# Performance work log

Hardware: AMD Instinct MI355X
Metric: run time of the kernel (lower is better)

## Reference

```python
import jax, jax.numpy as jnp
import numpy as np

B, N, HID, H, FFN, E = 1, 50000, 96, 8, 384, 800000
D = HID // H
SCALE = float(np.sqrt(D))


def _layernorm(x, g, b, eps=1e-5):
    mu = jnp.mean(x, axis=-1, keepdims=True)
    var = jnp.var(x, axis=-1, keepdims=True)
    return (x - mu) * jax.lax.rsqrt(var + eps) * g + b


def setup_inputs() -> dict:
    key = jax.random.key(0)
    ks = jax.random.split(key, 20)
    std = 0.02
    inp = {
        "x": jax.random.normal(ks[0], (B, N, HID), dtype=jnp.float32),
        "edge_index": jax.random.randint(ks[1], (2, E), 0, B * N, dtype=jnp.int32),
        "ln1_g": jnp.ones((HID,), jnp.float32),
        "ln1_b": jnp.zeros((HID,), jnp.float32),
        "Wq": jax.random.normal(ks[2], (HID, HID), jnp.float32) * std,
        "bq": jnp.zeros((HID,), jnp.float32),
        "Wk": jax.random.normal(ks[3], (HID, HID), jnp.float32) * std,
        "bk": jnp.zeros((HID,), jnp.float32),
        "Wv": jax.random.normal(ks[4], (HID, HID), jnp.float32) * std,
        "bv": jnp.zeros((HID,), jnp.float32),
        "Wo": jax.random.normal(ks[5], (HID, HID), jnp.float32) * std,
        "bo": jnp.zeros((HID,), jnp.float32),
        "ln2_g": jnp.ones((HID,), jnp.float32),
        "ln2_b": jnp.zeros((HID,), jnp.float32),
        "W1": jax.random.normal(ks[6], (HID, FFN), jnp.float32) * std,
        "b1": jnp.zeros((FFN,), jnp.float32),
        "W2": jax.random.normal(ks[7], (FFN, HID), jnp.float32) * std,
        "b2": jnp.zeros((HID,), jnp.float32),
    }
    return inp


def _sparse_attn(q, k, v, edge_index):
    # q,k,v: [B*N, H, D]; edge_index: [2, E]
    src_idx = edge_index[0].astype(jnp.int32)
    dst_idx = edge_index[1].astype(jnp.int32)
    src = k[src_idx]                                # [E, H, D]
    dest = q[dst_idx]                               # [E, H, D]
    score = jnp.sum(src * dest, axis=-1, keepdims=True) / SCALE  # [E, H, 1]
    score = jnp.exp(jnp.clip(score, -5.0, 5.0))
    msg = v[src_idx] * score                        # [E, H, D]
    wV = jax.ops.segment_sum(msg, dst_idx, num_segments=B * N)   # [B*N, H, D]
    Z = jax.ops.segment_sum(score, dst_idx, num_segments=B * N)  # [B*N, H, 1]
    return wV / (Z + 1e-6)


def reference(x, edge_index, ln1_g, ln1_b, Wq, bq, Wk, bk, Wv, bv, Wo, bo,
              ln2_g, ln2_b, W1, b1, W2, b2):
    # --- self-attention block ---
    y = _layernorm(x, ln1_g, ln1_b)                 # [B, N, HID]
    q = (y @ Wq + bq).reshape(B * N, H, D)
    k = (y @ Wk + bk).reshape(B * N, H, D)
    v = (y @ Wv + bv).reshape(B * N, H, D)
    a = _sparse_attn(q, k, v, edge_index)           # [B*N, H, D]
    a = a.reshape(B, N, HID)
    y = a @ Wo + bo
    x = x + y
    # --- FFN block ---
    y = _layernorm(x, ln2_g, ln2_b)
    y = jax.nn.gelu(y @ W1 + b1, approximate=False)
    y = y @ W2 + b2
    return x + y
```

## Files before the change

### kernel.cpp

```cpp
#include <hip/hip_runtime.h>
#include <hip/hip_bf16.h>
#include <math.h>

#define NN 50000
#define HIDD 96
#define NH 8
#define HD 12
#define FFND 384
#define NE 800000
#define NB 98
#define BSTRIDE 12288

#define INV_SCALE 0.28867513459481287f
#define LOG2E 1.4426950408889634f

typedef short short8 __attribute__((ext_vector_type(8)));
typedef float f32x4 __attribute__((ext_vector_type(4)));
typedef float f32x2 __attribute__((ext_vector_type(2)));

__device__ __forceinline__ float bf2f(unsigned short u) {
    union { unsigned int i; float f; } c;
    c.i = ((unsigned int)u) << 16;
    return c.f;
}

__global__ __launch_bounds__(256) void prep(
    int* __restrict__ gcursor,
    const float* __restrict__ Wq, const float* __restrict__ Wk,
    const float* __restrict__ Wv, const float* __restrict__ Wo,
    const float* __restrict__ W1, const float* __restrict__ W2,
    __hip_bfloat16* __restrict__ wbuf,
    const float* __restrict__ x, const float* __restrict__ g1,
    const float* __restrict__ b1, __hip_bfloat16* __restrict__ ybf) {
    int b = blockIdx.x;
    int t = threadIdx.x;
    if (b == 0) {
        if (t < 128) gcursor[t] = t * BSTRIDE;
        return;
    }
    if (b < 433) {
        int idx = b - 1;
        const float* W; __hip_bfloat16* D; int K, N; int i;
        if (idx < 144)      { W = W1; D = wbuf + 36864; K = 96;  N = 384; i = idx * 256 + t; }
        else if (idx < 288) { W = W2; D = wbuf + 73728; K = 384; N = 96;  i = (idx - 144) * 256 + t; }
        else {
            int slab = (idx - 288) / 36;
            W = (slab == 0) ? Wq : (slab == 1) ? Wk : (slab == 2) ? Wv : Wo;
            D = wbuf + slab * 9216; K = 96; N = 96;
            i = ((idx - 288) % 36) * 256 + t;
        }
        if (i < K * N) {
            int n = i / K, k = i % K;
            D[i] = __float2bfloat16(W[k * N + n]);
        }
    } else {
        int row = (b - 433) * 4 + (t >> 6);
        int lane = t & 63;
        if (row >= NN) return;
        const float* xr = x + (size_t)row * HIDD;
        float v0 = xr[lane];
        float v1 = (lane < 32) ? xr[64 + lane] : 0.0f;
        float s = v0 + v1, q = v0 * v0 + v1 * v1;
#pragma unroll
        for (int o = 32; o > 0; o >>= 1) {
            s += __shfl_xor(s, o);
            q += __shfl_xor(q, o);
        }
        float mean = s * (1.0f / 96.0f);
        float var = q * (1.0f / 96.0f) - mean * mean;
        float rs = rsqrtf(var + 1e-5f);
        __hip_bfloat16* yr = ybf + (size_t)row * HIDD;
        yr[lane] = __float2bfloat16((v0 - mean) * rs * g1[lane] + b1[lane]);
        if (lane < 32)
            yr[64 + lane] = __float2bfloat16((v1 - mean) * rs * g1[64 + lane] + b1[64 + lane]);
    }
}

__global__ __launch_bounds__(256) void scatter_qkv(
    const int* __restrict__ ei, int* __restrict__ gcursor,
    unsigned int* __restrict__ ebuf,
    const __hip_bfloat16* __restrict__ A, const __hip_bfloat16* __restrict__ wbuf,
    const float* __restrict__ bq, const float* __restrict__ bk,
    const float* __restrict__ bv,
    __hip_bfloat16* __restrict__ qbf, unsigned char* __restrict__ kv) {
    int b = blockIdx.x;
    int t = threadIdx.x;
    if (b < 391) {
        __shared__ int lcount[128];
        __shared__ int lbase[128];
        int e0 = b * 2048;
        if (t < 128) lcount[t] = 0;
        __syncthreads();
        int rank[8], dsts[8], srcv[8];
#pragma unroll
        for (int i = 0; i < 8; i++) {
            int e = e0 + t + i * 256;
            if (e < NE) {
                srcv[i] = ei[e];
                int d = ei[NE + e];
                dsts[i] = d;
                rank[i] = atomicAdd(&lcount[d >> 9], 1);
            } else dsts[i] = -1;
        }
        __syncthreads();
        if (t < 128) lbase[t] = lcount[t] ? atomicAdd(&gcursor[t], lcount[t]) : 0;
        __syncthreads();
#pragma unroll
        for (int i = 0; i < 8; i++) {
            if (dsts[i] >= 0) {
                int bk_ = dsts[i] >> 9;
                ebuf[lbase[bk_] + rank[i]] =
                    ((unsigned int)dsts[i] << 16) | (unsigned int)srcv[i];
            }
        }
    } else {
        __shared__ __hip_bfloat16 Bs[96][104];
        int xb = b - 391;
        int lane = t & 63, wave = t >> 6;
        int row0 = xb * 128 + wave * 32;
        int lr = lane & 15, kg = lane >> 4;
        bool val0 = (row0 + 16 <= NN);
        bool val1 = (row0 + 32 <= NN);
        int ra0 = val0 ? row0 : 0;
        int ra1 = val1 ? (row0 + 16) : 0;
        short8 a0[3], a1[3];
#pragma unroll
        for (int kc = 0; kc < 3; kc++) {
            a0[kc] = *(const short8*)&A[(size_t)(ra0 + lr) * 96 + kc * 32 + kg * 8];
            a1[kc] = *(const short8*)&A[(size_t)(ra1 + lr) * 96 + kc * 32 + kg * 8];
        }
        for (int y = 0; y < 3; y++) {
            const __hip_bfloat16* slab = wbuf + y * 9216;
            for (int i = t * 8; i < 96 * 96; i += 256 * 8) {
                int r = i / 96, c = i % 96;
                *(short8*)&Bs[r][c] = *(const short8*)&slab[r * 96 + c];
            }
            __syncthreads();
            f32x4 acc[2][6];
#pragma unroll
            for (int f = 0; f < 2; f++)
#pragma unroll
                for (int ct = 0; ct < 6; ct++) acc[f][ct] = (f32x4){0.f, 0.f, 0.f, 0.f};
#pragma unroll
            for (int kc = 0; kc < 3; kc++) {
#pragma unroll
                for (int ct = 0; ct < 6; ct++) {
                    short8 bf_ = *(const short8*)&Bs[ct * 16 + lr][kc * 32 + kg * 8];
                    acc[0][ct] = __builtin_amdgcn_mfma_f32_16x16x32_bf16(a0[kc], bf_, acc[0][ct], 0, 0, 0);
                    acc[1][ct] = __builtin_amdgcn_mfma_f32_16x16x32_bf16(a1[kc], bf_, acc[1][ct], 0, 0, 0);
                }
            }
            const float* bias = (y == 0) ? bq : (y == 1) ? bk : bv;
            int koff = (y == 2) ? 12 : 0;
#pragma unroll
            for (int f = 0; f < 2; f++) {
                if (f == 0 ? !val0 : !val1) continue;
                int crow = row0 + f * 16 + kg * 4;
#pragma unroll
                for (int ct = 0; ct < 6; ct++) {
                    int col = ct * 16 + lr;
                    float bb = bias[col];
#pragma unroll
                    for (int r = 0; r < 4; r++) {
                        float o = acc[f][ct][r] + bb;
                        if (y == 0) {
                            qbf[(size_t)(crow + r) * HIDD + col] = __float2bfloat16(o);
                        } else {
                            unsigned int enc =
                                (unsigned int)__builtin_amdgcn_cvt_pk_fp8_f32(o, o, 0, false);
                            kv[(size_t)(crow + r) * 192 + (col / 12) * 24 + koff + (col % 12)]
                                = (unsigned char)(enc & 0xffu);
                        }
                    }
                }
            }
            __syncthreads();
        }
    }
}

__global__ __launch_bounds__(1024) void bucket_build(
    const unsigned int* __restrict__ ebuf, const int* __restrict__ gcursor,
    uint2* __restrict__ rowrange, unsigned short* __restrict__ srcs) {
    __shared__ int cnt[512];
    int b = blockIdx.x;
    int t = threadIdx.x;
    int n0 = b * 512;
    int beg = b * BSTRIDE;
    int end = gcursor[b];
    if (t < 512) cnt[t] = 0;
    __syncthreads();
    for (int e = beg + t; e < end; e += 1024)
        atomicAdd(&cnt[(ebuf[e] >> 16) - n0], 1);
    __syncthreads();
    int my = (t < 512) ? cnt[t] : 0;
    for (int off = 1; off < 512; off <<= 1) {
        int v = (t >= off && t < 512) ? cnt[t - off] : 0;
        __syncthreads();
        if (t < 512) cnt[t] += v;
        __syncthreads();
    }
    int excl = (t > 0 && t < 512) ? cnt[t - 1] : 0;
    int base = beg + excl;
    if (t < 512 && n0 + t < NN)
        rowrange[n0 + t] = make_uint2((unsigned)base, (unsigned)(base + my));
    __syncthreads();
    if (t < 512) cnt[t] = base;
    __syncthreads();
    for (int e = beg + t; e < end; e += 1024) {
        unsigned int u = ebuf[e];
        int pos = atomicAdd(&cnt[(u >> 16) - n0], 1);
        srcs[pos] = (unsigned short)(u & 0xffffu);
    }
}

__global__ __launch_bounds__(256) void proj_ln(
    const __hip_bfloat16* __restrict__ A, const __hip_bfloat16* __restrict__ BT,
    const float* __restrict__ bias, const float* __restrict__ R,
    const float* __restrict__ g2, const float* __restrict__ b2v,
    __hip_bfloat16* __restrict__ x2, __hip_bfloat16* __restrict__ ybf) {
    constexpr int K = 96;
    __shared__ __hip_bfloat16 Bs[96][K + 8];
    int t = threadIdx.x;
    int lane = t & 63, wave = t >> 6;
    int row0 = blockIdx.x * 128 + wave * 32;
    int lr = lane & 15, kg = lane >> 4;
    bool val0 = (row0 + 16 <= NN);
    bool val1 = (row0 + 32 <= NN);
    int ra0 = val0 ? row0 : 0;
    int ra1 = val1 ? (row0 + 16) : 0;
    const __hip_bfloat16* A0 = A + (size_t)(ra0 + lr) * K + kg * 8;
    const __hip_bfloat16* A1 = A + (size_t)(ra1 + lr) * K + kg * 8;
    f32x4 acc[2][6];
#pragma unroll
    for (int f = 0; f < 2; f++)
#pragma unroll
        for (int ct = 0; ct < 6; ct++) acc[f][ct] = (f32x4){0.f, 0.f, 0.f, 0.f};

    for (int i = t * 8; i < 96 * K; i += 256 * 8) {
        int r = i / K, c = i % K;
        *(short8*)&Bs[r][c] = *(const short8*)&BT[(size_t)r * K + c];
    }
    __syncthreads();
#pragma unroll
    for (int kc = 0; kc < K; kc += 32) {
        short8 a0 = *(const short8*)(A0 + kc);
        short8 a1 = *(const short8*)(A1 + kc);
#pragma unroll
        for (int ct = 0; ct < 6; ct++) {
            short8 bf_ = *(const short8*)&Bs[ct * 16 + lr][kc + kg * 8];
            acc[0][ct] = __builtin_amdgcn_mfma_f32_16x16x32_bf16(a0, bf_, acc[0][ct], 0, 0, 0);
            acc[1][ct] = __builtin_amdgcn_mfma_f32_16x16x32_bf16(a1, bf_, acc[1][ct], 0, 0, 0);
        }
    }

    float bo_[6], gv[6], bv_[6];
#pragma unroll
    for (int ct = 0; ct < 6; ct++) {
        int col = ct * 16 + lr;
        bo_[ct] = bias[col];
        gv[ct]  = g2[col];
        bv_[ct] = b2v[col];
    }
#pragma unroll
    for (int f = 0; f < 2; f++) {
        if (f == 0 ? !val0 : !val1) continue;
        int crow = row0 + f * 16 + kg * 4;
#pragma unroll
        for (int r = 0; r < 4; r++) {
            int row = crow + r;
            float o[6], s1 = 0.f, s2 = 0.f;
#pragma unroll
            for (int ct = 0; ct < 6; ct++) {
                int col = ct * 16 + lr;
                float val = acc[f][ct][r] + bo_[ct] + R[(size_t)row * 96 + col];
                o[ct] = val; s1 += val; s2 += val * val;
            }
#pragma unroll
            for (int m = 1; m < 16; m <<= 1) {
                s1 += __shfl_xor(s1, m);
                s2 += __shfl_xor(s2, m);
            }
            float mu = s1 * (1.0f / 96.0f);
            float var = s2 * (1.0f / 96.0f) - mu * mu;
            float rs = rsqrtf(var + 1e-5f);
#pragma unroll
            for (int ct = 0; ct < 6; ct++) {
                int col = ct * 16 + lr;
                x2[(size_t)row * 96 + col] = __float2bfloat16(o[ct]);
                ybf[(size_t)row * 96 + col] =
                    __float2bfloat16((o[ct] - mu) * rs * gv[ct] + bv_[ct]);
            }
        }
    }
}

__global__ __launch_bounds__(256) void ffn1_p(
    const __hip_bfloat16* __restrict__ ybf, const __hip_bfloat16* __restrict__ W1T,
    const float* __restrict__ b1, __hip_bfloat16* __restrict__ hbf) {
    __shared__ __hip_bfloat16 Bs[96][104];
    int t = threadIdx.x, lane = t & 63, wave = t >> 6;
    int lr = lane & 15, kg = lane >> 4;
    int row0 = blockIdx.x * 64 + wave * 16;
    bool valid = (row0 + 16 <= NN);
    int ra = valid ? row0 : 0;
    short8 af[3];
#pragma unroll
    for (int kc = 0; kc < 3; kc++)
        af[kc] = *(const short8*)&ybf[(size_t)(ra + lr) * 96 + kc * 32 + kg * 8];

    for (int s = 0; s < 4; s++) {
        const __hip_bfloat16* slab = W1T + (size_t)s * 96 * 96;
        for (int i = t * 8; i < 96 * 96; i += 256 * 8) {
            int r = i / 96, c = i % 96;
            *(short8*)&Bs[r][c] = *(const short8*)&slab[r * 96 + c];
        }
        __syncthreads();
        f32x4 acc[6];
#pragma unroll
        for (int ct = 0; ct < 6; ct++) acc[ct] = (f32x4){0.f, 0.f, 0.f, 0.f};
#pragma unroll
        for (int kc = 0; kc < 3; kc++) {
#pragma unroll
            for (int ct = 0; ct < 6; ct++) {
                short8 bf_ = *(const short8*)&Bs[ct * 16 + lr][kc * 32 + kg * 8];
                acc[ct] = __builtin_amdgcn_mfma_f32_16x16x32_bf16(af[kc], bf_, acc[ct], 0, 0, 0);
            }
        }
        if (valid) {
            int crow = row0 + kg * 4;
#pragma unroll
            for (int ct = 0; ct < 6; ct++) {
                int col = s * 96 + ct * 16 + lr;
                float bb = b1[col];
#pragma unroll
                for (int r = 0; r < 4; r++) {
                    float o = acc[ct][r] + bb;
                    o = 0.5f * o * (1.0f + erff(o * 0.70710678118654752f));
                    hbf[(size_t)(crow + r) * FFND + col] = __float2bfloat16(o);
                }
            }
        }
        __syncthreads();
    }
}

__global__ __launch_bounds__(256) void ffn2_p(
    const __hip_bfloat16* __restrict__ hbf, const __hip_bfloat16* __restrict__ W2T,
    const float* __restrict__ b2v, const __hip_bfloat16* __restrict__ x2,
    float* __restrict__ out) {
    __shared__ __hip_bfloat16 Bs[4][48][104];
    int t = threadIdx.x, lane = t & 63, wave = t >> 6;
    int lr = lane & 15, kg = lane >> 4;
    int row0 = blockIdx.x * 64 + wave * 16;
    bool valid = (row0 + 16 <= NN);
    int ra = valid ? row0 : 0;
    short8 hf[12];
#pragma unroll
    for (int kc = 0; kc < 12; kc++)
        hf[kc] = *(const short8*)&hbf[(size_t)(ra + lr) * FFND + kc * 32 + kg * 8];

    for (int ch = 0; ch < 2; ch++) {
        const __hip_bfloat16* wslab = W2T + (size_t)ch * 48 * 384;
        for (int i = t * 8; i < 48 * 384; i += 256 * 8) {
            int r = i / 384, c = i % 384;
            *(short8*)&Bs[c / 96][r][c % 96] = *(const short8*)&wslab[(size_t)r * 384 + c];
        }
        __syncthreads();
        f32x4 acc[3];
#pragma unroll
        for (int ct = 0; ct < 3; ct++) acc[ct] = (f32x4){0.f, 0.f, 0.f, 0.f};
#pragma unroll
        for (int kc = 0; kc < 12; kc++) {
#pragma unroll
            for (int ct = 0; ct < 3; ct++) {
                short8 bf_ = *(const short8*)&Bs[kc / 3][ct * 16 + lr][(kc % 3) * 32 + kg * 8];
                acc[ct] = __builtin_amdgcn_mfma_f32_16x16x32_bf16(hf[kc], bf_, acc[ct], 0, 0, 0);
            }
        }
        if (valid) {
            int crow = row0 + kg * 4;
#pragma unroll
            for (int ct = 0; ct < 3; ct++) {
                int col = ch * 48 + ct * 16 + lr;
                float bb = b2v[col];
#pragma unroll
                for (int r = 0; r < 4; r++) {
                    float o = acc[ct][r] + bb
                            + __bfloat162float(x2[(size_t)(crow + r) * 96 + col]);
                    out[(size_t)(crow + r) * 96 + col] = o;
                }
            }
        }
        __syncthreads();
    }
}

__global__ __launch_bounds__(256) void attn_gather(
    const __hip_bfloat16* __restrict__ qbf, const unsigned char* __restrict__ kv,
    const uint2* __restrict__ rowrange, const unsigned short* __restrict__ srcs,
    __hip_bfloat16* __restrict__ abf) {
    int wave = (blockIdx.x * blockDim.x + threadIdx.x) >> 6;
    int lane = threadIdx.x & 63;
    if (wave >= NN) return;
    int dst = wave;
    int h = lane & 7;
    int eslot = lane >> 3;
    float qf[12];
    {
        const uint2* qp = (const uint2*)(qbf + (size_t)dst * HIDD + h * HD);
        uint2 u0 = qp[0], u1 = qp[1], u2 = qp[2];
        unsigned int w[6] = {u0.x, u0.y, u1.x, u1.y, u2.x, u2.y};
#pragma unroll
        for (int i = 0; i < 6; i++) {
            qf[2 * i]     = bf2f((unsigned short)(w[i] & 0xffffu));
            qf[2 * i + 1] = bf2f((unsigned short)(w[i] >> 16));
        }
    }
    uint2 rr = rowrange[dst];
    int beg = (int)rr.x, end = (int)rr.y;
    float acc[12];
#pragma unroll
    for (int i = 0; i < 12; i++) acc[i] = 0.0f;
    float zz = 0.0f;

    int e = beg + eslot;
    bool has = e < end;
    uint2 cA, cB, cC;
    if (has) {
        int src = (int)srcs[e];
        const uint2* kp = (const uint2*)(kv + (size_t)src * 192 + h * 24);
        cA = kp[0]; cB = kp[1]; cC = kp[2];
    }
    while (has) {
        int en = e + 8;
        bool hasn = en < end;
        uint2 nA, nB, nC;
        if (hasn) {
            int srcn = (int)srcs[en];
            const uint2* kp = (const uint2*)(kv + (size_t)srcn * 192 + h * 24);
            nA = kp[0]; nB = kp[1]; nC = kp[2];
        }
        f32x2 p;
        float dot = 0.0f;
        p = __builtin_amdgcn_cvt_pk_f32_fp8(cA.x, false); dot += p[0] * qf[0]  + p[1] * qf[1];
        p = __builtin_amdgcn_cvt_pk_f32_fp8(cA.x, true);  dot += p[0] * qf[2]  + p[1] * qf[3];
        p = __builtin_amdgcn_cvt_pk_f32_fp8(cA.y, false); dot += p[0] * qf[4]  + p[1] * qf[5];
        p = __builtin_amdgcn_cvt_pk_f32_fp8(cA.y, true);  dot += p[0] * qf[6]  + p[1] * qf[7];
        p = __builtin_amdgcn_cvt_pk_f32_fp8(cB.x, false); dot += p[0] * qf[8]  + p[1] * qf[9];
        p = __builtin_amdgcn_cvt_pk_f32_fp8(cB.x, true);  dot += p[0] * qf[10] + p[1] * qf[11];
        float s = fminf(fmaxf(dot * INV_SCALE, -5.0f), 5.0f);
        float sc = exp2f(s * LOG2E);
        p = __builtin_amdgcn_cvt_pk_f32_fp8(cB.y, false); acc[0]  += p[0] * sc; acc[1]  += p[1] * sc;
        p = __builtin_amdgcn_cvt_pk_f32_fp8(cB.y, true);  acc[2]  += p[0] * sc; acc[3]  += p[1] * sc;
        p = __builtin_amdgcn_cvt_pk_f32_fp8(cC.x, false); acc[4]  += p[0] * sc; acc[5]  += p[1] * sc;
        p = __builtin_amdgcn_cvt_pk_f32_fp8(cC.x, true);  acc[6]  += p[0] * sc; acc[7]  += p[1] * sc;
        p = __builtin_amdgcn_cvt_pk_f32_fp8(cC.y, false); acc[8]  += p[0] * sc; acc[9]  += p[1] * sc;
        p = __builtin_amdgcn_cvt_pk_f32_fp8(cC.y, true);  acc[10] += p[0] * sc; acc[11] += p[1] * sc;
        zz += sc;
        cA = nA; cB = nB; cC = nC;
        e = en; has = hasn;
    }
#pragma unroll
    for (int m = 8; m < 64; m <<= 1) {
#pragma unroll
        for (int i = 0; i < 12; i++) acc[i] += __shfl_xor(acc[i], m);
        zz += __shfl_xor(zz, m);
    }
    if (eslot == 0) {
        float inv = 1.0f / (zz + 1e-6f);
        __hip_bfloat16* ar = abf + (size_t)dst * HIDD + h * HD;
#pragma unroll
        for (int i = 0; i < 12; i++) ar[i] = __float2bfloat16(acc[i] * inv);
    }
}

extern "C" void kernel_launch(void* const* d_in, const int* in_sizes, int n_in,
                              void* d_out, int out_size, void* d_ws, size_t ws_size,
                              hipStream_t stream) {
    const float* x     = (const float*)d_in[0];
    const int*   ei    = (const int*)d_in[1];
    const float* ln1_g = (const float*)d_in[2];
    const float* ln1_b = (const float*)d_in[3];
    const float* Wq    = (const float*)d_in[4];
    const float* bq    = (const float*)d_in[5];
    const float* Wk    = (const float*)d_in[6];
    const float* bk    = (const float*)d_in[7];
    const float* Wv    = (const float*)d_in[8];
    const float* bv    = (const float*)d_in[9];
    const float* Wo    = (const float*)d_in[10];
    const float* bo    = (const float*)d_in[11];
    const float* ln2_g = (const float*)d_in[12];
    const float* ln2_b = (const float*)d_in[13];
    const float* W1    = (const float*)d_in[14];
    const float* b1    = (const float*)d_in[15];
    const float* W2    = (const float*)d_in[16];
    const float* b2    = (const float*)d_in[17];
    float* out = (float*)d_out;

    float* ws = (float*)d_ws;
    const size_t NF = (size_t)NN * HIDD;
    __hip_bfloat16* qbf = (__hip_bfloat16*)ws;
    unsigned char*  kv  = (unsigned char*)(ws + NF / 2);
    __hip_bfloat16* abf = (__hip_bfloat16*)(ws + NF / 2 + NF);
    __hip_bfloat16* hbf = (__hip_bfloat16*)ws;
    __hip_bfloat16* x2  = (__hip_bfloat16*)(ws + 2 * NF);
    __hip_bfloat16* ybf = (__hip_bfloat16*)(ws + 2 * NF + NF / 2);
    int* ibase = (int*)(ws + 3 * NF);
    uint2* rowrange = (uint2*)ibase;
    unsigned short* srcs = (unsigned short*)(ibase + 2 * NN);
    int* gcursor = ibase + 2 * NN + (NB * BSTRIDE + 1) / 2;
    unsigned int* ebuf = (unsigned int*)(gcursor + 128);
    __hip_bfloat16* wbuf = (__hip_bfloat16*)(ws + 3 * NF + NF / 2);
    __hip_bfloat16* WoT = wbuf + 27648;
    __hip_bfloat16* W1T = wbuf + 36864;
    __hip_bfloat16* W2T = wbuf + 73728;

    const int MT = (NN + 127) / 128;
    const int FT = (NN + 63) / 64;

    prep<<<433 + 12500, 256, 0, stream>>>(gcursor, Wq, Wk, Wv, Wo, W1, W2, wbuf,
                                          x, ln1_g, ln1_b, ybf);
    scatter_qkv<<<391 + MT, 256, 0, stream>>>(ei, gcursor, ebuf,
                                              ybf, wbuf, bq, bk, bv, qbf, kv);
    bucket_build<<<NB, 1024, 0, stream>>>(ebuf, gcursor, rowrange, srcs);
    attn_gather<<<(NN + 3) / 4, 256, 0, stream>>>(qbf, kv, rowrange, srcs, abf);
    proj_ln<<<MT, 256, 0, stream>>>(abf, WoT, bo, x, ln2_g, ln2_b, x2, ybf);
    ffn1_p<<<FT, 256, 0, stream>>>(ybf, W1T, b1, hbf);
    ffn2_p<<<FT, 256, 0, stream>>>(hbf, W2T, b2, x2, out);
}
```

Measured before the change: 134.1 us.

## Regroup pipeline stages and store FFN hidden activations as fp8

The edge scatter moves into the prep kernel, and the bucket build is merged with the QKV projection into one 512-thread kernel. This drops a launch, and the QKV GEMM can overlap with the bucket build. The gcursor init becomes a memset with relative offsets. The FFN hidden activations are now written as fp8 and expanded to bf16 in ffn2, which halves that intermediate traffic at the cost of lower precision.

```diff
diff --git a/kernel.cpp b/kernel.cpp
--- a/kernel.cpp
+++ b/kernel.cpp
@@ -24,8 +24,26 @@
     return c.f;
 }
 
-__global__ __launch_bounds__(256) void prep(
-    int* __restrict__ gcursor,
+__device__ __forceinline__ short f2bf_exact(float f) {
+    return (short)(__float_as_uint(f) >> 16);
+}
+
+__device__ __forceinline__ short8 fp8x8_to_bf16x8(uint2 u) {
+    f32x2 p0 = __builtin_amdgcn_cvt_pk_f32_fp8(u.x, false);
+    f32x2 p1 = __builtin_amdgcn_cvt_pk_f32_fp8(u.x, true);
+    f32x2 p2 = __builtin_amdgcn_cvt_pk_f32_fp8(u.y, false);
+    f32x2 p3 = __builtin_amdgcn_cvt_pk_f32_fp8(u.y, true);
+    short8 r;
+    r[0] = f2bf_exact(p0[0]); r[1] = f2bf_exact(p0[1]);
+    r[2] = f2bf_exact(p1[0]); r[3] = f2bf_exact(p1[1]);
+    r[4] = f2bf_exact(p2[0]); r[5] = f2bf_exact(p2[1]);
+    r[6] = f2bf_exact(p3[0]); r[7] = f2bf_exact(p3[1]);
+    return r;
+}
+
+__global__ __launch_bounds__(256) void prep2(
+    const int* __restrict__ ei, int* __restrict__ gcursor,
+    unsigned int* __restrict__ ebuf,
     const float* __restrict__ Wq, const float* __restrict__ Wk,
     const float* __restrict__ Wv, const float* __restrict__ Wo,
     const float* __restrict__ W1, const float* __restrict__ W2,
@@ -34,12 +52,36 @@
     const float* __restrict__ b1, __hip_bfloat16* __restrict__ ybf) {
     int b = blockIdx.x;
     int t = threadIdx.x;
-    if (b == 0) {
-        if (t < 128) gcursor[t] = t * BSTRIDE;
-        return;
-    }
-    if (b < 433) {
-        int idx = b - 1;
+    if (b < 391) {
+        __shared__ int lcount[128];
+        __shared__ int lbase[128];
+        int e0 = b * 2048;
+        if (t < 128) lcount[t] = 0;
+        __syncthreads();
+        int rank[8], dsts[8], srcv[8];
+#pragma unroll
+        for (int i = 0; i < 8; i++) {
+            int e = e0 + t + i * 256;
+            if (e < NE) {
+                srcv[i] = ei[e];
+                int d = ei[NE + e];
+                dsts[i] = d;
+                rank[i] = atomicAdd(&lcount[d >> 9], 1);
+            } else dsts[i] = -1;
+        }
+        __syncthreads();
+        if (t < 128) lbase[t] = lcount[t] ? atomicAdd(&gcursor[t], lcount[t]) : 0;
+        __syncthreads();
+#pragma unroll
+        for (int i = 0; i < 8; i++) {
+            if (dsts[i] >= 0) {
+                int bk_ = dsts[i] >> 9;
+                ebuf[bk_ * BSTRIDE + lbase[bk_] + rank[i]] =
+                    ((unsigned int)dsts[i] << 16) | (unsigned int)srcv[i];
+            }
+        }
+    } else if (b < 823) {
+        int idx = b - 391;
         const float* W; __hip_bfloat16* D; int K, N; int i;
         if (idx < 144)      { W = W1; D = wbuf + 36864; K = 96;  N = 384; i = idx * 256 + t; }
         else if (idx < 288) { W = W2; D = wbuf + 73728; K = 384; N = 96;  i = (idx - 144) * 256 + t; }
@@ -54,7 +96,7 @@
             D[i] = __float2bfloat16(W[k * N + n]);
         }
     } else {
-        int row = (b - 433) * 4 + (t >> 6);
+        int row = (b - 823) * 4 + (t >> 6);
         int lane = t & 63;
         if (row >= NN) return;
         const float* xr = x + (size_t)row * HIDD;
@@ -76,93 +118,85 @@
     }
 }
 
-__global__ __launch_bounds__(256) void scatter_qkv(
-    const int* __restrict__ ei, int* __restrict__ gcursor,
-    unsigned int* __restrict__ ebuf,
+__global__ __launch_bounds__(512) void build_qkv(
+    const unsigned int* __restrict__ ebuf, const int* __restrict__ gcursor,
+    uint2* __restrict__ rowrange, unsigned short* __restrict__ srcs,
     const __hip_bfloat16* __restrict__ A, const __hip_bfloat16* __restrict__ wbuf,
     const float* __restrict__ bq, const float* __restrict__ bk,
     const float* __restrict__ bv,
     __hip_bfloat16* __restrict__ qbf, unsigned char* __restrict__ kv) {
+    __shared__ int cnt[512];
+    __shared__ __hip_bfloat16 Bs[96][104];
     int b = blockIdx.x;
     int t = threadIdx.x;
-    if (b < 391) {
-        __shared__ int lcount[128];
-        __shared__ int lbase[128];
-        int e0 = b * 2048;
-        if (t < 128) lcount[t] = 0;
-        __syncthreads();
-        int rank[8], dsts[8], srcv[8];
-#pragma unroll
-        for (int i = 0; i < 8; i++) {
-            int e = e0 + t + i * 256;
-            if (e < NE) {
-                srcv[i] = ei[e];
-                int d = ei[NE + e];
-                dsts[i] = d;
-                rank[i] = atomicAdd(&lcount[d >> 9], 1);
-            } else dsts[i] = -1;
-        }
-        __syncthreads();
-        if (t < 128) lbase[t] = lcount[t] ? atomicAdd(&gcursor[t], lcount[t]) : 0;
-        __syncthreads();
-#pragma unroll
-        for (int i = 0; i < 8; i++) {
-            if (dsts[i] >= 0) {
-                int bk_ = dsts[i] >> 9;
-                ebuf[lbase[bk_] + rank[i]] =
-                    ((unsigned int)dsts[i] << 16) | (unsigned int)srcv[i];
-            }
+    if (b < NB) {
+        int n0 = b * 512;
+        int beg = b * BSTRIDE;
+        int end = beg + gcursor[b];
+        cnt[t] = 0;
+        __syncthreads();
+        for (int e = beg + t; e < end; e += 512)
+            atomicAdd(&cnt[(ebuf[e] >> 16) - n0], 1);
+        __syncthreads();
+        int my = cnt[t];
+        for (int off = 1; off < 512; off <<= 1) {
+            int v = (t >= off) ? cnt[t - off] : 0;
+            __syncthreads();
+            cnt[t] += v;
+            __syncthreads();
+        }
+        int excl = (t > 0) ? cnt[t - 1] : 0;
+        int base = beg + excl;
+        if (n0 + t < NN)
+            rowrange[n0 + t] = make_uint2((unsigned)base, (unsigned)(base + my));
+        __syncthreads();
+        cnt[t] = base;
+        __syncthreads();
+        for (int e = beg + t; e < end; e += 512) {
+            unsigned int u = ebuf[e];
+            int pos = atomicAdd(&cnt[(u >> 16) - n0], 1);
+            srcs[pos] = (unsigned short)(u & 0xffffu);
         }
     } else {
-        __shared__ __hip_bfloat16 Bs[96][104];
-        int xb = b - 391;
+        int xb = b - NB;
         int lane = t & 63, wave = t >> 6;
-        int row0 = xb * 128 + wave * 32;
+        int row0 = xb * 128 + wave * 16;
         int lr = lane & 15, kg = lane >> 4;
-        bool val0 = (row0 + 16 <= NN);
-        bool val1 = (row0 + 32 <= NN);
-        int ra0 = val0 ? row0 : 0;
-        int ra1 = val1 ? (row0 + 16) : 0;
-        short8 a0[3], a1[3];
-#pragma unroll
-        for (int kc = 0; kc < 3; kc++) {
-            a0[kc] = *(const short8*)&A[(size_t)(ra0 + lr) * 96 + kc * 32 + kg * 8];
-            a1[kc] = *(const short8*)&A[(size_t)(ra1 + lr) * 96 + kc * 32 + kg * 8];
-        }
+        bool valid = (row0 + 16 <= NN);
+        int ra = valid ? row0 : 0;
+        short8 af[3];
+#pragma unroll
+        for (int kc = 0; kc < 3; kc++)
+            af[kc] = *(const short8*)&A[(size_t)(ra + lr) * 96 + kc * 32 + kg * 8];
         for (int y = 0; y < 3; y++) {
             const __hip_bfloat16* slab = wbuf + y * 9216;
-            for (int i = t * 8; i < 96 * 96; i += 256 * 8) {
+            for (int i = t * 8; i < 96 * 96; i += 512 * 8) {
                 int r = i / 96, c = i % 96;
                 *(short8*)&Bs[r][c] = *(const short8*)&slab[r * 96 + c];
             }
             __syncthreads();
-            f32x4 acc[2][6];
-#pragma unroll
-            for (int f = 0; f < 2; f++)
-#pragma unroll
-                for (int ct = 0; ct < 6; ct++) acc[f][ct] = (f32x4){0.f, 0.f, 0.f, 0.f};
+            f32x4 acc[6];
+#pragma unroll
+            for (int ct = 0; ct < 6; ct++) acc[ct] = (f32x4){0.f, 0.f, 0.f, 0.f};
 #pragma unroll
             for (int kc = 0; kc < 3; kc++) {
 #pragma unroll
                 for (int ct = 0; ct < 6; ct++) {
                     short8 bf_ = *(const short8*)&Bs[ct * 16 + lr][kc * 32 + kg * 8];
-                    acc[0][ct] = __builtin_amdgcn_mfma_f32_16x16x32_bf16(a0[kc], bf_, acc[0][ct], 0, 0, 0);
-                    acc[1][ct] = __builtin_amdgcn_mfma_f32_16x16x32_bf16(a1[kc], bf_, acc[1][ct], 0, 0, 0);
+                    acc[ct] = __builtin_amdgcn_mfma_f32_16x16x32_bf16(af[kc], bf_, acc[ct], 0, 0, 0);
                 }
             }
-            const float* bias = (y == 0) ? bq : (y == 1) ? bk : bv;
-            int koff = (y == 2) ? 12 : 0;
-#pragma unroll
-            for (int f = 0; f < 2; f++) {
-                if (f == 0 ? !val0 : !val1) continue;
-                int crow = row0 + f * 16 + kg * 4;
+            if (valid) {
+                const float* bias = (y == 0) ? bq : (y == 1) ? bk : bv;
+                int koff = (y == 2) ? 12 : 0;
+                int crow = row0 + kg * 4;
 #pragma unroll
                 for (int ct = 0; ct < 6; ct++) {
                     int col = ct * 16 + lr;
                     float bb = bias[col];
 #pragma unroll
                     for (int r = 0; r < 4; r++) {
-                        float o = acc[f][ct][r] + bb;
+                        float o = acc[ct][r] + bb;
                         if (y == 0) {
                             qbf[(size_t)(crow + r) * HIDD + col] = __float2bfloat16(o);
                         } else {
@@ -176,41 +210,6 @@
             }
             __syncthreads();
         }
-    }
-}
-
-__global__ __launch_bounds__(1024) void bucket_build(
-    const unsigned int* __restrict__ ebuf, const int* __restrict__ gcursor,
-    uint2* __restrict__ rowrange, unsigned short* __restrict__ srcs) {
-    __shared__ int cnt[512];
-    int b = blockIdx.x;
-    int t = threadIdx.x;
-    int n0 = b * 512;
-    int beg = b * BSTRIDE;
-    int end = gcursor[b];
-    if (t < 512) cnt[t] = 0;
-    __syncthreads();
-    for (int e = beg + t; e < end; e += 1024)
-        atomicAdd(&cnt[(ebuf[e] >> 16) - n0], 1);
-    __syncthreads();
-    int my = (t < 512) ? cnt[t] : 0;
-    for (int off = 1; off < 512; off <<= 1) {
-        int v = (t >= off && t < 512) ? cnt[t - off] : 0;
-        __syncthreads();
-        if (t < 512) cnt[t] += v;
-        __syncthreads();
-    }
-    int excl = (t > 0 && t < 512) ? cnt[t - 1] : 0;
-    int base = beg + excl;
-    if (t < 512 && n0 + t < NN)
-        rowrange[n0 + t] = make_uint2((unsigned)base, (unsigned)(base + my));
-    __syncthreads();
-    if (t < 512) cnt[t] = base;
-    __syncthreads();
-    for (int e = beg + t; e < end; e += 1024) {
-        unsigned int u = ebuf[e];
-        int pos = atomicAdd(&cnt[(u >> 16) - n0], 1);
-        srcs[pos] = (unsigned short)(u & 0xffffu);
     }
 }
 
@@ -297,7 +296,7 @@
 
 __global__ __launch_bounds__(256) void ffn1_p(
     const __hip_bfloat16* __restrict__ ybf, const __hip_bfloat16* __restrict__ W1T,
-    const float* __restrict__ b1, __hip_bfloat16* __restrict__ hbf) {
+    const float* __restrict__ b1, unsigned char* __restrict__ hbf8) {
     __shared__ __hip_bfloat16 Bs[96][104];
     int t = threadIdx.x, lane = t & 63, wave = t >> 6;
     int lr = lane & 15, kg = lane >> 4;
@@ -337,7 +336,9 @@
                 for (int r = 0; r < 4; r++) {
                     float o = acc[ct][r] + bb;
                     o = 0.5f * o * (1.0f + erff(o * 0.70710678118654752f));
-                    hbf[(size_t)(crow + r) * FFND + col] = __float2bfloat16(o);
+                    unsigned int enc =
+                        (unsigned int)__builtin_amdgcn_cvt_pk_fp8_f32(o, o, 0, false);
+                    hbf8[(size_t)(crow + r) * FFND + col] = (unsigned char)(enc & 0xffu);
                 }
             }
         }
@@ -346,7 +347,7 @@
 }
 
 __global__ __launch_bounds__(256) void ffn2_p(
-    const __hip_bfloat16* __restrict__ hbf, const __hip_bfloat16* __restrict__ W2T,
+    const unsigned char* __restrict__ hbf8, const __hip_bfloat16* __restrict__ W2T,
     const float* __restrict__ b2v, const __hip_bfloat16* __restrict__ x2,
     float* __restrict__ out) {
     __shared__ __hip_bfloat16 Bs[4][48][104];
@@ -355,10 +356,11 @@
     int row0 = blockIdx.x * 64 + wave * 16;
     bool valid = (row0 + 16 <= NN);
     int ra = valid ? row0 : 0;
+    const unsigned char* H = hbf8 + (size_t)(ra + lr) * FFND + kg * 8;
     short8 hf[12];
 #pragma unroll
     for (int kc = 0; kc < 12; kc++)
-        hf[kc] = *(const short8*)&hbf[(size_t)(ra + lr) * FFND + kc * 32 + kg * 8];
+        hf[kc] = fp8x8_to_bf16x8(*(const uint2*)(H + kc * 32));
 
     for (int ch = 0; ch < 2; ch++) {
         const __hip_bfloat16* wslab = W2T + (size_t)ch * 48 * 384;
@@ -503,7 +505,7 @@
     __hip_bfloat16* qbf = (__hip_bfloat16*)ws;
     unsigned char*  kv  = (unsigned char*)(ws + NF / 2);
     __hip_bfloat16* abf = (__hip_bfloat16*)(ws + NF / 2 + NF);
-    __hip_bfloat16* hbf = (__hip_bfloat16*)ws;
+    unsigned char*  hbf8 = (unsigned char*)ws;
     __hip_bfloat16* x2  = (__hip_bfloat16*)(ws + 2 * NF);
     __hip_bfloat16* ybf = (__hip_bfloat16*)(ws + 2 * NF + NF / 2);
     int* ibase = (int*)(ws + 3 * NF);
@@ -519,13 +521,14 @@
     const int MT = (NN + 127) / 128;
     const int FT = (NN + 63) / 64;
 
-    prep<<<433 + 12500, 256, 0, stream>>>(gcursor, Wq, Wk, Wv, Wo, W1, W2, wbuf,
-                                          x, ln1_g, ln1_b, ybf);
-    scatter_qkv<<<391 + MT, 256, 0, stream>>>(ei, gcursor, ebuf,
-                                              ybf, wbuf, bq, bk, bv, qbf, kv);
-    bucket_build<<<NB, 1024, 0, stream>>>(ebuf, gcursor, rowrange, srcs);
+    hipMemsetAsync(gcursor, 0, 128 * sizeof(int), stream);
+    prep2<<<823 + 12500, 256, 0, stream>>>(ei, gcursor, ebuf,
+                                           Wq, Wk, Wv, Wo, W1, W2, wbuf,
+                                           x, ln1_g, ln1_b, ybf);
+    build_qkv<<<NB + MT, 512, 0, stream>>>(ebuf, gcursor, rowrange, srcs,
+                                           ybf, wbuf, bq, bk, bv, qbf, kv);
     attn_gather<<<(NN + 3) / 4, 256, 0, stream>>>(qbf, kv, rowrange, srcs, abf);
     proj_ln<<<MT, 256, 0, stream>>>(abf, WoT, bo, x, ln2_g, ln2_b, x2, ybf);
-    ffn1_p<<<FT, 256, 0, stream>>>(ybf, W1T, b1, hbf);
-    ffn2_p<<<FT, 256, 0, stream>>>(hbf, W2T, b2, x2, out);
-}
+    ffn1_p<<<FT, 256, 0, stream>>>(ybf, W1T, b1, hbf8);
+    ffn2_p<<<FT, 256, 0, stream>>>(hbf8, W2T, b2, x2, out);
+}
```

Result: faster. 126.8 us (median of 2 runs) (-5.5%).
